# Kernel tuning notes

Hardware: AMD Instinct MI355X
Metric: run time of the kernel (lower is better)

Reference implementation:

```python
import jax, jax.numpy as jnp
import numpy as np

B, N, H, DH, E, D_IN = 2, 2048, 8, 32, 65536, 256
O = H * DH
SCALE = float(np.sqrt(DH))


def setup_inputs() -> dict:
    key = jax.random.key(0)
    ks = jax.random.split(key, 8)
    rng = np.random.default_rng(0)
    x = jax.random.normal(ks[0], (B, N, D_IN), jnp.float32)
    adj = jax.random.uniform(ks[1], (B, N, N), jnp.float32)
    # unique edges per graph so scatter-add matches torch advanced-index +=
    flat = np.stack([rng.choice(N * N, size=E, replace=False) for _ in range(B)])
    edge_index = jnp.asarray(np.stack([flat // N, flat % N], axis=1), jnp.int32)  # [B,2,E]
    edge_attr = jax.random.normal(ks[2], (B, E, H), jnp.float32)
    mask = jnp.ones((B, N), dtype=bool)
    qkv_w = jax.random.normal(ks[3], (D_IN, 3 * O), jnp.float32) / np.sqrt(D_IN)
    qkv_b = jnp.zeros((3 * O,), jnp.float32)
    e_w1 = jax.random.normal(ks[4], (H, H), jnp.float32) / np.sqrt(H)
    e_b1 = jnp.zeros((H,), jnp.float32)
    e_w2 = jax.random.normal(ks[5], (H, H), jnp.float32) / np.sqrt(H)
    e_b2 = jnp.zeros((H,), jnp.float32)
    shifts = jnp.asarray(np.linspace(0.1, 0.8, H), jnp.float32).reshape(1, H, 1, 1)
    widths = jnp.full((1, H, 1, 1), 0.5, jnp.float32)
    self_loop_W = jnp.asarray(1.0 / DH + rng.uniform(0, 1, H), jnp.float32).reshape(1, H, 1, 1)
    return dict(x=x, adj=adj, edge_attr=edge_attr, qkv_w=qkv_w, qkv_b=qkv_b,
                e_w1=e_w1, e_b1=e_b1, e_w2=e_w2, e_b2=e_b2,
                shifts=shifts, widths=widths, self_loop_W=self_loop_W,
                edge_index=edge_index, mask=mask)


def reference(x, adj, edge_attr, qkv_w, qkv_b, e_w1, e_b1, e_w2, e_b2,
              shifts, widths, self_loop_W, edge_index, mask):
    Bq, Nq = x.shape[0], x.shape[1]
    # qkv projection -> [3,B,H,N,DH]
    qkv = (x @ qkv_w + qkv_b).reshape(Bq, Nq, 3, H, DH)
    qkv = jnp.transpose(qkv, (2, 0, 3, 1, 4))
    Q, K, V = qkv[0], qkv[1], qkv[2]
    # edge FFN applied twice (eval mode: noise/dropout are identity)
    def ffn(e):
        return jax.nn.relu(e @ e_w1 + e_b1) @ e_w2 + e_b2
    ea = ffn(ffn(edge_attr))                      # [B,E,H]
    ea = jnp.transpose(ea, (0, 2, 1))             # [B,H,E]
    # scores + learned moire adjacency bias
    scores = jnp.einsum('bhqd,bhkd->bhqk', Q, K) / SCALE
    moire = jnp.exp(-((adj[:, None] - shifts) ** 2) / (2.0 * widths ** 2))  # gaussian focus
    moire = jnp.clip(moire, 1e-6, None)
    s = scores + jnp.log(moire)                   # [B,H,N,N]
    # scatter edge features into score matrix
    u = edge_index[:, 0, :]                        # [B,E]
    v = edge_index[:, 1, :]
    bi = jnp.arange(Bq)[:, None, None]
    hi = jnp.arange(H)[None, :, None]
    s = s.at[bi, hi, u[:, None, :], v[:, None, :]].add(ea)
    # self-loop diagonal bias (non-trainable)
    s = s + jnp.eye(Nq, dtype=s.dtype)[None, None] * self_loop_W
    # mask and softmax
    m2 = mask[:, None, :] & mask[:, :, None]       # [B,N,N]
    s = jnp.where(m2[:, None], s, jnp.asarray(-1e6, s.dtype))
    attn = jax.nn.softmax(s, axis=-1)
    out = jnp.einsum('bhqk,bhkd->bhqd', attn, V)
    return jnp.transpose(out, (0, 2, 1, 3)).reshape(Bq, Nq, O)
```

## Files before the change

### kernel.cpp

```cpp
#include <hip/hip_runtime.h>

#define B_ 2
#define N_ 2048
#define H_ 8
#define DH_ 32
#define E_ 65536
#define DIN_ 256
#define KT 256
#define NKT (N_ / KT)
#define ECAP 32
#define QSCALE 0.2550348872f
#define LOG2E 1.4426950408889634f
#define LOG2MIN -19.931568569324174f

typedef short bf16x8 __attribute__((ext_vector_type(8)));
typedef float floatx4 __attribute__((ext_vector_type(4)));

__device__ __forceinline__ unsigned short f2b(float f){
  union { float f; unsigned int u; } v; v.f = f;
  return (unsigned short)((v.u + 0x7fffu + ((v.u >> 16) & 1u)) >> 16);
}
__device__ __forceinline__ bf16x8 f8_to_bf(const float* p){
  float4 a = *(const float4*)p, b = *(const float4*)(p + 4);
  bf16x8 r;
  r[0] = (short)f2b(a.x); r[1] = (short)f2b(a.y); r[2] = (short)f2b(a.z); r[3] = (short)f2b(a.w);
  r[4] = (short)f2b(b.x); r[5] = (short)f2b(b.y); r[6] = (short)f2b(b.z); r[7] = (short)f2b(b.w);
  return r;
}
__device__ __forceinline__ unsigned int cvt_pk_bf16(float lo, float hi){
  unsigned int r;
  asm("v_cvt_pk_bf16_f32 %0, %1, %2" : "=v"(r) : "v"(lo), "v"(hi));
  return r;
}
__device__ __forceinline__ float fexp2(float x){
  float r;
  asm("v_exp_f32 %0, %1" : "=v"(r) : "v"(x));
  return r;
}

__global__ __launch_bounds__(256) void prep_kernel(
    const float* __restrict__ eattr,
    const float* __restrict__ w1, const float* __restrict__ b1,
    const float* __restrict__ w2, const float* __restrict__ b2,
    float* __restrict__ ea,
    const int* __restrict__ ei, int* __restrict__ cnt, unsigned int* __restrict__ pck,
    const float* __restrict__ w, unsigned short* __restrict__ wT,
    const float* __restrict__ x, unsigned short* __restrict__ xb)
{
  int bb = blockIdx.x, tid = threadIdx.x;
  if (bb < 512){
    __shared__ float W1[64], W2[64], Bv1[8], Bv2[8];
    if (tid < 64){ W1[tid] = w1[tid]; W2[tid] = w2[tid]; }
    if (tid < 8){ Bv1[tid] = b1[tid]; Bv2[tid] = b2[tid]; }
    __syncthreads();
    int gid = bb * 256 + tid;
    const float* ep = eattr + (size_t)gid * 8;
    float cur[8];
#pragma unroll
    for (int i = 0; i < 8; ++i) cur[i] = ep[i];
#pragma unroll
    for (int pass = 0; pass < 2; ++pass){
      float t[8];
#pragma unroll
      for (int j = 0; j < 8; ++j){
        float s = Bv1[j];
#pragma unroll
        for (int i = 0; i < 8; ++i) s += cur[i] * W1[i * 8 + j];
        t[j] = fmaxf(s, 0.f);
      }
#pragma unroll
      for (int j = 0; j < 8; ++j){
        float s = Bv2[j];
#pragma unroll
        for (int i = 0; i < 8; ++i) s += t[i] * W2[i * 8 + j];
        cur[j] = s;
      }
    }
    float* op = ea + (size_t)gid * 8;
#pragma unroll
    for (int j = 0; j < 8; ++j) op[j] = cur[j] * LOG2E;
  } else if (bb < 1024){
    int gid = (bb - 512) * 256 + tid;
    int b = gid >> 16, e = gid & (E_ - 1);
    int u = ei[(size_t)b * 2 * E_ + e];
    int v = ei[(size_t)b * 2 * E_ + E_ + e];
    int bucket = ((b << 11) + u) * 8 + (v >> 8);
    int slot = atomicAdd(&cnt[bucket], 1);
    if (slot < ECAP) pck[(size_t)bucket * ECAP + slot] = ((unsigned int)e << 11) | (unsigned int)v;
  } else if (bb < 1280){
    int k = bb - 1024;
    for (int c = tid; c < 768; c += 256)
      wT[(size_t)c * 256 + k] = f2b(w[(size_t)k * 768 + c]);
  } else {
    int gid = (bb - 1280) * 256 + tid;
    bf16x8 v = f8_to_bf(x + (size_t)gid * 8);
    *(bf16x8*)(xb + (size_t)gid * 8) = v;
  }
}

__global__ __launch_bounds__(256) void qkv_kernel(
    const unsigned short* __restrict__ xb, const unsigned short* __restrict__ wT,
    const float* __restrict__ bias,
    unsigned short* __restrict__ Qb, unsigned short* __restrict__ Kb, unsigned short* __restrict__ Vt)
{
  int tid = threadIdx.x;
  int wave = tid >> 6, lane = tid & 63, m = lane & 15, quad = lane >> 4;
  int rowbase = blockIdx.x * 16;
  int colbase = blockIdx.y * 64 + wave * 16;
  floatx4 acc = {0.f, 0.f, 0.f, 0.f};
#pragma unroll
  for (int kb = 0; kb < 8; ++kb){
    bf16x8 af = *(const bf16x8*)(xb + (size_t)(rowbase + m) * DIN_ + kb * 32 + quad * 8);
    bf16x8 bf = *(const bf16x8*)(wT + (size_t)(colbase + m) * DIN_ + kb * 32 + quad * 8);
    acc = __builtin_amdgcn_mfma_f32_16x16x32_bf16(af, bf, acc, 0, 0, 0);
  }
  int ccol = colbase + m;
  int which = ccol >> 8, hh = (ccol >> 5) & 7, dh = ccol & 31;
  float bv = bias[ccol];
  int row0 = rowbase + quad * 4;
  int bidx = row0 >> 11, n0 = row0 & (N_ - 1);
  size_t bh = (size_t)(bidx * H_ + hh);
  if (which == 0){
#pragma unroll
    for (int r = 0; r < 4; ++r)
      Qb[(bh * N_ + n0 + r) * DH_ + dh] = f2b((acc[r] + bv) * QSCALE);
  } else if (which == 1){
#pragma unroll
    for (int r = 0; r < 4; ++r)
      Kb[(bh * N_ + n0 + r) * DH_ + dh] = f2b(acc[r] + bv);
  } else {
    ushort4 st;
    st.x = f2b(acc[0] + bv); st.y = f2b(acc[1] + bv);
    st.z = f2b(acc[2] + bv); st.w = f2b(acc[3] + bv);
    *(ushort4*)(Vt + (bh * DH_ + dh) * N_ + n0) = st;
  }
}

__global__ __launch_bounds__(128) void attn_kernel(
    const unsigned short* __restrict__ Qb, const unsigned short* __restrict__ Kb,
    const unsigned short* __restrict__ Vt, const float* __restrict__ adj,
    const float* __restrict__ ea, const int* __restrict__ cnt, const unsigned int* __restrict__ pck,
    const float* __restrict__ shifts, const float* __restrict__ widths,
    const float* __restrict__ selfW, float* __restrict__ out)
{
  __shared__ float S[2][16][260];

  int bid = blockIdx.x;
  int xcd = bid & 7, t = bid >> 3;
  int hp = t & 3;
  int bqt = xcd * 32 + (t >> 2);
  int b = bqt >> 7, qt = bqt & 127;
  int qbase = qt * 16;
  int tid = threadIdx.x, wave = tid >> 6, lane = tid & 63, m = lane & 15, quad = lane >> 4;
  int h = hp * 2 + wave;
  float shift_h = shifts[h];
  float w_h = widths[h];
  float i2w_h = LOG2E / (2.f * w_h * w_h);
  float selfW_h = selfW[h] * LOG2E;
  size_t krow = (size_t)(b * H_ + h) * N_;
  size_t vrow = (size_t)(b * H_ + h) * DH_;
  bf16x8 qfrag = *(const bf16x8*)(Qb + (krow + qbase + m) * DH_ + quad * 8);
  float (*Sw)[260] = S[wave];

  int rr = lane >> 2, sl0 = lane & 3;
  const int* cntp = cnt + ((size_t)(b * N_) + qbase + rr) * 8;
  const unsigned int* pckp = pck + ((size_t)((b * N_ + qbase + rr) * 8)) * ECAP;
  const float* eabase = ea + (size_t)b * E_ * H_ + h;
  const float* adjp = adj + ((size_t)b * N_ + qbase + m) * N_ + quad * 8;
  const unsigned short* vp0 = Vt + (vrow + m) * N_ + quad * 8;
  const unsigned short* vp1 = Vt + (vrow + 16 + m) * N_ + quad * 8;
  const unsigned short* kp  = Kb + (krow + m) * DH_ + quad * 8;

  floatx4 sh4 = {shift_h, shift_h, shift_h, shift_h};
  floatx4 ni4 = {-i2w_h, -i2w_h, -i2w_h, -i2w_h};
  floatx4 lm4 = {LOG2MIN, LOG2MIN, LOG2MIN, LOG2MIN};
  floatx4 z4  = {0.f, 0.f, 0.f, 0.f};

  float mcur = -1e30f, lcur = 0.f;
  floatx4 oacc0 = z4, oacc1 = z4;

  int nb_c = cntp[0]; nb_c = nb_c > ECAP ? ECAP : nb_c;
  unsigned int pk0 = pckp[sl0];
  unsigned int pk1 = pckp[sl0 + 4];
  int vv0_c = (int)(pk0 & (N_ - 1));
  int vv1_c = (int)(pk1 & (N_ - 1));
  bool g0_c = (sl0 < nb_c);
  bool g1_c = (sl0 + 4 < nb_c);
  float ea0_c = 0.f, ea1_c = 0.f;
  if (g0_c) ea0_c = eabase[(size_t)(pk0 >> 11) * H_];
  if (g1_c) ea1_c = eabase[(size_t)(pk1 >> 11) * H_];

#pragma unroll 2
  for (int kt = 0; kt < NKT; ++kt){
    int k0 = kt * KT;
    int nb_n = 0; unsigned int pk0_n = 0, pk1_n = 0;
    if (kt + 1 < NKT){
      nb_n  = cntp[kt + 1];
      pk0_n = pckp[(kt + 1) * ECAP + sl0];
      pk1_n = pckp[(kt + 1) * ECAP + sl0 + 4];
    }
#pragma unroll
    for (int cb = 0; cb < 4; ++cb){
      const unsigned short* kpb = kp + (size_t)(k0 + cb * 64) * DH_;
#pragma unroll
      for (int s = 0; s < 4; ++s){
        bf16x8 kf = *(const bf16x8*)(kpb + (size_t)(s * 16) * DH_);
        floatx4 acc = __builtin_amdgcn_mfma_f32_16x16x32_bf16(qfrag, kf, z4, 0, 0, 0);
#pragma unroll
        for (int r = 0; r < 4; ++r)
          Sw[quad * 4 + r][cb * 64 + s * 16 + m] = acc[r];
      }
    }
    {
      int dw = qbase - k0;
      if ((unsigned)dw < 256u && lane < 16)
        Sw[lane][dw + lane] += selfW_h;
    }
    if (g0_c) Sw[rr][vv0_c - k0] += ea0_c;
    if (g1_c) Sw[rr][vv1_c - k0] += ea1_c;
    if (nb_c > 8){
      for (int slot = sl0 + 8; slot < nb_c; slot += 4){
        unsigned int p = pckp[kt * ECAP + slot];
        Sw[rr][(int)(p & (N_ - 1)) - k0] += eabase[(size_t)(p >> 11) * H_];
      }
    }
    int vv0_n = 0, vv1_n = 0; bool g0_n = false, g1_n = false;
    float ea0_n = 0.f, ea1_n = 0.f;
    if (kt + 1 < NKT){
      nb_n = nb_n > ECAP ? ECAP : nb_n;
      vv0_n = (int)(pk0_n & (N_ - 1));
      vv1_n = (int)(pk1_n & (N_ - 1));
      g0_n = (sl0 < nb_n);
      g1_n = (sl0 + 4 < nb_n);
      if (g0_n) ea0_n = eabase[(size_t)(pk0_n >> 11) * H_];
      if (g1_n) ea1_n = eabase[(size_t)(pk1_n >> 11) * H_];
    }
    floatx4 sv[4][4];
#pragma unroll
    for (int cb = 0; cb < 4; ++cb){
      const float* sp = &Sw[m][cb * 64 + quad * 8];
      sv[cb][0] = *(const floatx4*)(sp);
      sv[cb][1] = *(const floatx4*)(sp + 4);
      sv[cb][2] = *(const floatx4*)(sp + 32);
      sv[cb][3] = *(const floatx4*)(sp + 36);
      const float* ap = adjp + k0 + cb * 64;
      floatx4 a0 = *(const floatx4*)(ap);
      floatx4 a1 = *(const floatx4*)(ap + 4);
      floatx4 a2 = *(const floatx4*)(ap + 32);
      floatx4 a3 = *(const floatx4*)(ap + 36);
      floatx4 d;
      d = a0 - sh4; sv[cb][0] += __builtin_elementwise_max(d * d * ni4, lm4);
      d = a1 - sh4; sv[cb][1] += __builtin_elementwise_max(d * d * ni4, lm4);
      d = a2 - sh4; sv[cb][2] += __builtin_elementwise_max(d * d * ni4, lm4);
      d = a3 - sh4; sv[cb][3] += __builtin_elementwise_max(d * d * ni4, lm4);
    }
    floatx4 mx01 = __builtin_elementwise_max(
        __builtin_elementwise_max(sv[0][0], sv[0][1]),
        __builtin_elementwise_max(sv[0][2], sv[0][3]));
    floatx4 mx23 = __builtin_elementwise_max(
        __builtin_elementwise_max(sv[1][0], sv[1][1]),
        __builtin_elementwise_max(sv[1][2], sv[1][3]));
    floatx4 mx45 = __builtin_elementwise_max(
        __builtin_elementwise_max(sv[2][0], sv[2][1]),
        __builtin_elementwise_max(sv[2][2], sv[2][3]));
    floatx4 mx67 = __builtin_elementwise_max(
        __builtin_elementwise_max(sv[3][0], sv[3][1]),
        __builtin_elementwise_max(sv[3][2], sv[3][3]));
    floatx4 mxv = __builtin_elementwise_max(__builtin_elementwise_max(mx01, mx23),
                                            __builtin_elementwise_max(mx45, mx67));
    float lm = fmaxf(fmaxf(mxv.x, mxv.y), fmaxf(mxv.z, mxv.w));
    lm = fmaxf(lm, __shfl_xor(lm, 16));
    lm = fmaxf(lm, __shfl_xor(lm, 32));
    float mnew = fmaxf(mcur, lm);
    float al = fexp2(mcur - mnew);
    mcur = mnew;
    float al0 = __shfl(al, quad * 4 + 0);
    float al1 = __shfl(al, quad * 4 + 1);
    float al2 = __shfl(al, quad * 4 + 2);
    float al3 = __shfl(al, quad * 4 + 3);
    oacc0[0] *= al0; oacc0[1] *= al1; oacc0[2] *= al2; oacc0[3] *= al3;
    oacc1[0] *= al0; oacc1[1] *= al1; oacc1[2] *= al2; oacc1[3] *= al3;
    floatx4 m4 = {mcur, mcur, mcur, mcur};
    floatx4 psv = z4;
#pragma unroll
    for (int cb = 0; cb < 4; ++cb){
      const unsigned short* vA = vp0 + k0 + cb * 64;
      const unsigned short* vB = vp1 + k0 + cb * 64;
      bf16x8 vf00 = *(const bf16x8*)(vA);
      bf16x8 vf01 = *(const bf16x8*)(vB);
      bf16x8 vf10 = *(const bf16x8*)(vA + 32);
      bf16x8 vf11 = *(const bf16x8*)(vB + 32);
      floatx4 e0 = sv[cb][0] - m4, e1 = sv[cb][1] - m4;
      floatx4 e2 = sv[cb][2] - m4, e3 = sv[cb][3] - m4;
      floatx4 p0, p1, p2, p3;
      p0.x = fexp2(e0.x); p0.y = fexp2(e0.y); p0.z = fexp2(e0.z); p0.w = fexp2(e0.w);
      p1.x = fexp2(e1.x); p1.y = fexp2(e1.y); p1.z = fexp2(e1.z); p1.w = fexp2(e1.w);
      p2.x = fexp2(e2.x); p2.y = fexp2(e2.y); p2.z = fexp2(e2.z); p2.w = fexp2(e2.w);
      p3.x = fexp2(e3.x); p3.y = fexp2(e3.y); p3.z = fexp2(e3.z); p3.w = fexp2(e3.w);
      psv += (p0 + p1) + (p2 + p3);
      union { bf16x8 v; unsigned int u[4]; } PL, PH;
      PL.u[0] = cvt_pk_bf16(p0.x, p0.y); PL.u[1] = cvt_pk_bf16(p0.z, p0.w);
      PL.u[2] = cvt_pk_bf16(p1.x, p1.y); PL.u[3] = cvt_pk_bf16(p1.z, p1.w);
      PH.u[0] = cvt_pk_bf16(p2.x, p2.y); PH.u[1] = cvt_pk_bf16(p2.z, p2.w);
      PH.u[2] = cvt_pk_bf16(p3.x, p3.y); PH.u[3] = cvt_pk_bf16(p3.z, p3.w);
      oacc0 = __builtin_amdgcn_mfma_f32_16x16x32_bf16(PL.v, vf00, oacc0, 0, 0, 0);
      oacc1 = __builtin_amdgcn_mfma_f32_16x16x32_bf16(PL.v, vf01, oacc1, 0, 0, 0);
      oacc0 = __builtin_amdgcn_mfma_f32_16x16x32_bf16(PH.v, vf10, oacc0, 0, 0, 0);
      oacc1 = __builtin_amdgcn_mfma_f32_16x16x32_bf16(PH.v, vf11, oacc1, 0, 0, 0);
    }
    float ps = (psv.x + psv.y) + (psv.z + psv.w);
    ps += __shfl_xor(ps, 16);
    ps += __shfl_xor(ps, 32);
    lcur = lcur * al + ps;
    nb_c = nb_n; g0_c = g0_n; g1_c = g1_n;
    vv0_c = vv0_n; vv1_c = vv1_n; ea0_c = ea0_n; ea1_c = ea1_n;
  }

  float linv0 = 1.f / __shfl(lcur, quad * 4 + 0);
  float linv1 = 1.f / __shfl(lcur, quad * 4 + 1);
  float linv2 = 1.f / __shfl(lcur, quad * 4 + 2);
  float linv3 = 1.f / __shfl(lcur, quad * 4 + 3);
  float* ob = out + ((size_t)b * N_ + qbase + quad * 4) * (H_ * DH_) + h * DH_;
  ob[0 * H_ * DH_ + m]      = oacc0[0] * linv0;
  ob[0 * H_ * DH_ + 16 + m] = oacc1[0] * linv0;
  ob[1 * H_ * DH_ + m]      = oacc0[1] * linv1;
  ob[1 * H_ * DH_ + 16 + m] = oacc1[1] * linv1;
  ob[2 * H_ * DH_ + m]      = oacc0[2] * linv2;
  ob[2 * H_ * DH_ + 16 + m] = oacc1[2] * linv2;
  ob[3 * H_ * DH_ + m]      = oacc0[3] * linv3;
  ob[3 * H_ * DH_ + 16 + m] = oacc1[3] * linv3;
}

extern "C" void kernel_launch(void* const* d_in, const int* in_sizes, int n_in,
                              void* d_out, int out_size, void* d_ws, size_t ws_size,
                              hipStream_t stream)
{
  const float* x      = (const float*)d_in[0];
  const float* adj    = (const float*)d_in[1];
  const float* eattr  = (const float*)d_in[2];
  const float* qkvw   = (const float*)d_in[3];
  const float* qkvb   = (const float*)d_in[4];
  const float* ew1    = (const float*)d_in[5];
  const float* eb1    = (const float*)d_in[6];
  const float* ew2    = (const float*)d_in[7];
  const float* eb2    = (const float*)d_in[8];
  const float* shifts = (const float*)d_in[9];
  const float* widths = (const float*)d_in[10];
  const float* selfW  = (const float*)d_in[11];
  const int*   ei     = (const int*)d_in[12];
  float* out = (float*)d_out;

  char* ws = (char*)d_ws;
  unsigned short* Qb  = (unsigned short*)(ws);
  unsigned short* Kb  = (unsigned short*)(ws + ((size_t)2 << 20));
  unsigned short* Vt  = (unsigned short*)(ws + ((size_t)4 << 20));
  unsigned short* wT  = (unsigned short*)(ws + ((size_t)6 << 20));
  float*          ea  = (float*)(ws + ((size_t)7 << 20));
  int*            cnt = (int*)(ws + ((size_t)11 << 20));
  unsigned int*  pck  = (unsigned int*)(ws + ((size_t)12 << 20));
  unsigned short* xb  = (unsigned short*)(ws + ((size_t)16 << 20));

  hipMemsetAsync(cnt, 0, (size_t)B_ * N_ * 8 * sizeof(int), stream);
  hipLaunchKernelGGL(prep_kernel, dim3(1792), dim3(256), 0, stream,
                     eattr, ew1, eb1, ew2, eb2, ea, ei, cnt, pck, qkvw, wT, x, xb);
  hipLaunchKernelGGL(qkv_kernel, dim3(256, 12), dim3(256), 0, stream, xb, wT, qkvb, Qb, Kb, Vt);
  hipLaunchKernelGGL(attn_kernel, dim3(B_ * (H_ / 2) * (N_ / 16)), dim3(128), 0, stream,
                     Qb, Kb, Vt, adj, ea, cnt, pck, shifts, widths, selfW, out);
}
```

Baseline: 210.1 us.

## Split key range across two waves per head with flash-decoding style merge

Each block now runs four waves instead of two, so each head's key sequence is split into two halves processed by separate waves. The partial max, sum and output are merged through shared memory after a block barrier. To fit four waves, the per-wave score scratch is halved to 128 columns and each 256-key tile is processed in two sub-passes. This doubles the parallelism per query tile and shortens each wave's serial loop, at the cost of a final reduction, a barrier, and recomputation of the edge-slot filter per sub-pass.

```diff
diff --git a/kernel.cpp b/kernel.cpp
--- a/kernel.cpp
+++ b/kernel.cpp
@@ -7,7 +7,6 @@
 #define E_ 65536
 #define DIN_ 256
 #define KT 256
-#define NKT (N_ / KT)
 #define ECAP 32
 #define QSCALE 0.2550348872f
 #define LOG2E 1.4426950408889634f
@@ -136,14 +135,15 @@
   }
 }
 
-__global__ __launch_bounds__(128) void attn_kernel(
+__global__ __launch_bounds__(256) void attn_kernel(
     const unsigned short* __restrict__ Qb, const unsigned short* __restrict__ Kb,
     const unsigned short* __restrict__ Vt, const float* __restrict__ adj,
     const float* __restrict__ ea, const int* __restrict__ cnt, const unsigned int* __restrict__ pck,
     const float* __restrict__ shifts, const float* __restrict__ widths,
     const float* __restrict__ selfW, float* __restrict__ out)
 {
-  __shared__ float S[2][16][260];
+  __shared__ float S[4][16][132];
+  __shared__ float mfin[4][16], lfin[4][16];
 
   int bid = blockIdx.x;
   int xcd = bid & 7, t = bid >> 3;
@@ -152,7 +152,8 @@
   int b = bqt >> 7, qt = bqt & 127;
   int qbase = qt * 16;
   int tid = threadIdx.x, wave = tid >> 6, lane = tid & 63, m = lane & 15, quad = lane >> 4;
-  int h = hp * 2 + wave;
+  int hs = wave & 1, kh = wave >> 1;
+  int h = hp * 2 + hs;
   float shift_h = shifts[h];
   float w_h = widths[h];
   float i2w_h = LOG2E / (2.f * w_h * w_h);
@@ -160,7 +161,7 @@
   size_t krow = (size_t)(b * H_ + h) * N_;
   size_t vrow = (size_t)(b * H_ + h) * DH_;
   bf16x8 qfrag = *(const bf16x8*)(Qb + (krow + qbase + m) * DH_ + quad * 8);
-  float (*Sw)[260] = S[wave];
+  float (*Sw)[132] = S[wave];
 
   int rr = lane >> 2, sl0 = lane & 3;
   const int* cntp = cnt + ((size_t)(b * N_) + qbase + rr) * 8;
@@ -179,9 +180,10 @@
   float mcur = -1e30f, lcur = 0.f;
   floatx4 oacc0 = z4, oacc1 = z4;
 
-  int nb_c = cntp[0]; nb_c = nb_c > ECAP ? ECAP : nb_c;
-  unsigned int pk0 = pckp[sl0];
-  unsigned int pk1 = pckp[sl0 + 4];
+  int ktg0 = kh * 4;
+  int nb_c = cntp[ktg0]; nb_c = nb_c > ECAP ? ECAP : nb_c;
+  unsigned int pk0 = pckp[ktg0 * ECAP + sl0];
+  unsigned int pk1 = pckp[ktg0 * ECAP + sl0 + 4];
   int vv0_c = (int)(pk0 & (N_ - 1));
   int vv1_c = (int)(pk1 & (N_ - 1));
   bool g0_c = (sl0 < nb_c);
@@ -190,43 +192,68 @@
   if (g0_c) ea0_c = eabase[(size_t)(pk0 >> 11) * H_];
   if (g1_c) ea1_c = eabase[(size_t)(pk1 >> 11) * H_];
 
-#pragma unroll 2
-  for (int kt = 0; kt < NKT; ++kt){
-    int k0 = kt * KT;
+  for (int kt = 0; kt < 4; ++kt){
+    int ktg = ktg0 + kt;
+    int k0 = ktg * KT;
     int nb_n = 0; unsigned int pk0_n = 0, pk1_n = 0;
-    if (kt + 1 < NKT){
-      nb_n  = cntp[kt + 1];
-      pk0_n = pckp[(kt + 1) * ECAP + sl0];
-      pk1_n = pckp[(kt + 1) * ECAP + sl0 + 4];
-    }
-#pragma unroll
-    for (int cb = 0; cb < 4; ++cb){
-      const unsigned short* kpb = kp + (size_t)(k0 + cb * 64) * DH_;
-#pragma unroll
-      for (int s = 0; s < 4; ++s){
-        bf16x8 kf = *(const bf16x8*)(kpb + (size_t)(s * 16) * DH_);
-        floatx4 acc = __builtin_amdgcn_mfma_f32_16x16x32_bf16(qfrag, kf, z4, 0, 0, 0);
-#pragma unroll
-        for (int r = 0; r < 4; ++r)
-          Sw[quad * 4 + r][cb * 64 + s * 16 + m] = acc[r];
-      }
-    }
-    {
-      int dw = qbase - k0;
-      if ((unsigned)dw < 256u && lane < 16)
-        Sw[lane][dw + lane] += selfW_h;
-    }
-    if (g0_c) Sw[rr][vv0_c - k0] += ea0_c;
-    if (g1_c) Sw[rr][vv1_c - k0] += ea1_c;
-    if (nb_c > 8){
-      for (int slot = sl0 + 8; slot < nb_c; slot += 4){
-        unsigned int p = pckp[kt * ECAP + slot];
-        Sw[rr][(int)(p & (N_ - 1)) - k0] += eabase[(size_t)(p >> 11) * H_];
+    if (kt + 1 < 4){
+      nb_n  = cntp[ktg + 1];
+      pk0_n = pckp[(ktg + 1) * ECAP + sl0];
+      pk1_n = pckp[(ktg + 1) * ECAP + sl0 + 4];
+    }
+    floatx4 sv[4][4];
+#pragma unroll
+    for (int p = 0; p < 2; ++p){
+      int kw = k0 + p * 128;
+#pragma unroll
+      for (int cb = 0; cb < 2; ++cb){
+        const unsigned short* kpb = kp + (size_t)(kw + cb * 64) * DH_;
+#pragma unroll
+        for (int s = 0; s < 4; ++s){
+          bf16x8 kf = *(const bf16x8*)(kpb + (size_t)(s * 16) * DH_);
+          floatx4 acc = __builtin_amdgcn_mfma_f32_16x16x32_bf16(qfrag, kf, z4, 0, 0, 0);
+#pragma unroll
+          for (int r = 0; r < 4; ++r)
+            Sw[quad * 4 + r][cb * 64 + s * 16 + m] = acc[r];
+        }
+      }
+      {
+        int dw = qbase - kw;
+        if ((unsigned)dw < 128u && lane < 16)
+          Sw[lane][dw + lane] += selfW_h;
+      }
+      if (g0_c && ((vv0_c - k0) >> 7) == p) Sw[rr][(vv0_c - k0) & 127] += ea0_c;
+      if (g1_c && ((vv1_c - k0) >> 7) == p) Sw[rr][(vv1_c - k0) & 127] += ea1_c;
+      if (nb_c > 8){
+        for (int slot = sl0 + 8; slot < nb_c; slot += 4){
+          unsigned int pkx = pckp[ktg * ECAP + slot];
+          int c = (int)(pkx & (N_ - 1)) - k0;
+          if ((c >> 7) == p) Sw[rr][c & 127] += eabase[(size_t)(pkx >> 11) * H_];
+        }
+      }
+#pragma unroll
+      for (int cb = 0; cb < 2; ++cb){
+        int g = p * 2 + cb;
+        const float* sp = &Sw[m][cb * 64 + quad * 8];
+        sv[g][0] = *(const floatx4*)(sp);
+        sv[g][1] = *(const floatx4*)(sp + 4);
+        sv[g][2] = *(const floatx4*)(sp + 32);
+        sv[g][3] = *(const floatx4*)(sp + 36);
+        const float* ap = adjp + kw + cb * 64;
+        floatx4 a0 = *(const floatx4*)(ap);
+        floatx4 a1 = *(const floatx4*)(ap + 4);
+        floatx4 a2 = *(const floatx4*)(ap + 32);
+        floatx4 a3 = *(const floatx4*)(ap + 36);
+        floatx4 d;
+        d = a0 - sh4; sv[g][0] += __builtin_elementwise_max(d * d * ni4, lm4);
+        d = a1 - sh4; sv[g][1] += __builtin_elementwise_max(d * d * ni4, lm4);
+        d = a2 - sh4; sv[g][2] += __builtin_elementwise_max(d * d * ni4, lm4);
+        d = a3 - sh4; sv[g][3] += __builtin_elementwise_max(d * d * ni4, lm4);
       }
     }
     int vv0_n = 0, vv1_n = 0; bool g0_n = false, g1_n = false;
     float ea0_n = 0.f, ea1_n = 0.f;
-    if (kt + 1 < NKT){
+    if (kt + 1 < 4){
       nb_n = nb_n > ECAP ? ECAP : nb_n;
       vv0_n = (int)(pk0_n & (N_ - 1));
       vv1_n = (int)(pk1_n & (N_ - 1));
@@ -234,25 +261,6 @@
       g1_n = (sl0 + 4 < nb_n);
       if (g0_n) ea0_n = eabase[(size_t)(pk0_n >> 11) * H_];
       if (g1_n) ea1_n = eabase[(size_t)(pk1_n >> 11) * H_];
-    }
-    floatx4 sv[4][4];
-#pragma unroll
-    for (int cb = 0; cb < 4; ++cb){
-      const float* sp = &Sw[m][cb * 64 + quad * 8];
-      sv[cb][0] = *(const floatx4*)(sp);
-      sv[cb][1] = *(const floatx4*)(sp + 4);
-      sv[cb][2] = *(const floatx4*)(sp + 32);
-      sv[cb][3] = *(const floatx4*)(sp + 36);
-      const float* ap = adjp + k0 + cb * 64;
-      floatx4 a0 = *(const floatx4*)(ap);
-      floatx4 a1 = *(const floatx4*)(ap + 4);
-      floatx4 a2 = *(const floatx4*)(ap + 32);
-      floatx4 a3 = *(const floatx4*)(ap + 36);
-      floatx4 d;
-      d = a0 - sh4; sv[cb][0] += __builtin_elementwise_max(d * d * ni4, lm4);
-      d = a1 - sh4; sv[cb][1] += __builtin_elementwise_max(d * d * ni4, lm4);
-      d = a2 - sh4; sv[cb][2] += __builtin_elementwise_max(d * d * ni4, lm4);
-      d = a3 - sh4; sv[cb][3] += __builtin_elementwise_max(d * d * ni4, lm4);
     }
     floatx4 mx01 = __builtin_elementwise_max(
         __builtin_elementwise_max(sv[0][0], sv[0][1]),
@@ -268,10 +276,10 @@
         __builtin_elementwise_max(sv[3][2], sv[3][3]));
     floatx4 mxv = __builtin_elementwise_max(__builtin_elementwise_max(mx01, mx23),
                                             __builtin_elementwise_max(mx45, mx67));
-    float lm = fmaxf(fmaxf(mxv.x, mxv.y), fmaxf(mxv.z, mxv.w));
-    lm = fmaxf(lm, __shfl_xor(lm, 16));
-    lm = fmaxf(lm, __shfl_xor(lm, 32));
-    float mnew = fmaxf(mcur, lm);
+    float lmx = fmaxf(fmaxf(mxv.x, mxv.y), fmaxf(mxv.z, mxv.w));
+    lmx = fmaxf(lmx, __shfl_xor(lmx, 16));
+    lmx = fmaxf(lmx, __shfl_xor(lmx, 32));
+    float mnew = fmaxf(mcur, lmx);
     float al = fexp2(mcur - mnew);
     mcur = mnew;
     float al0 = __shfl(al, quad * 4 + 0);
@@ -283,15 +291,15 @@
     floatx4 m4 = {mcur, mcur, mcur, mcur};
     floatx4 psv = z4;
 #pragma unroll
-    for (int cb = 0; cb < 4; ++cb){
-      const unsigned short* vA = vp0 + k0 + cb * 64;
-      const unsigned short* vB = vp1 + k0 + cb * 64;
+    for (int g = 0; g < 4; ++g){
+      const unsigned short* vA = vp0 + k0 + g * 64;
+      const unsigned short* vB = vp1 + k0 + g * 64;
       bf16x8 vf00 = *(const bf16x8*)(vA);
       bf16x8 vf01 = *(const bf16x8*)(vB);
       bf16x8 vf10 = *(const bf16x8*)(vA + 32);
       bf16x8 vf11 = *(const bf16x8*)(vB + 32);
-      floatx4 e0 = sv[cb][0] - m4, e1 = sv[cb][1] - m4;
-      floatx4 e2 = sv[cb][2] - m4, e3 = sv[cb][3] - m4;
+      floatx4 e0 = sv[g][0] - m4, e1 = sv[g][1] - m4;
+      floatx4 e2 = sv[g][2] - m4, e3 = sv[g][3] - m4;
       floatx4 p0, p1, p2, p3;
       p0.x = fexp2(e0.x); p0.y = fexp2(e0.y); p0.z = fexp2(e0.z); p0.w = fexp2(e0.w);
       p1.x = fexp2(e1.x); p1.y = fexp2(e1.y); p1.z = fexp2(e1.z); p1.w = fexp2(e1.w);
@@ -316,19 +324,25 @@
     vv0_c = vv0_n; vv1_c = vv1_n; ea0_c = ea0_n; ea1_c = ea1_n;
   }
 
-  float linv0 = 1.f / __shfl(lcur, quad * 4 + 0);
-  float linv1 = 1.f / __shfl(lcur, quad * 4 + 1);
-  float linv2 = 1.f / __shfl(lcur, quad * 4 + 2);
-  float linv3 = 1.f / __shfl(lcur, quad * 4 + 3);
-  float* ob = out + ((size_t)b * N_ + qbase + quad * 4) * (H_ * DH_) + h * DH_;
-  ob[0 * H_ * DH_ + m]      = oacc0[0] * linv0;
-  ob[0 * H_ * DH_ + 16 + m] = oacc1[0] * linv0;
-  ob[1 * H_ * DH_ + m]      = oacc0[1] * linv1;
-  ob[1 * H_ * DH_ + 16 + m] = oacc1[1] * linv1;
-  ob[2 * H_ * DH_ + m]      = oacc0[2] * linv2;
-  ob[2 * H_ * DH_ + 16 + m] = oacc1[2] * linv2;
-  ob[3 * H_ * DH_ + m]      = oacc0[3] * linv3;
-  ob[3 * H_ * DH_ + 16 + m] = oacc1[3] * linv3;
+  if (quad == 0){ mfin[wave][m] = mcur; lfin[wave][m] = lcur; }
+  float* Ow = &S[wave][0][0];
+#pragma unroll
+  for (int r = 0; r < 4; ++r){
+    Ow[(quad * 4 + r) * 132 + m]      = oacc0[r];
+    Ow[(quad * 4 + r) * 132 + 16 + m] = oacc1[r];
+  }
+  __syncthreads();
+#pragma unroll
+  for (int ii = 0; ii < 4; ++ii){
+    int i = tid + ii * 256;
+    int hs2 = i >> 9, r = (i >> 5) & 15, d = i & 31;
+    float m0 = mfin[hs2][r], m1 = mfin[hs2 + 2][r];
+    float mg = fmaxf(m0, m1);
+    float w0 = fexp2(m0 - mg), w1 = fexp2(m1 - mg);
+    float o = S[hs2][r][d] * w0 + S[hs2 + 2][r][d] * w1;
+    float l = lfin[hs2][r] * w0 + lfin[hs2 + 2][r] * w1;
+    out[((size_t)b * N_ + qbase + r) * (H_ * DH_) + (hp * 2 + hs2) * DH_ + d] = o / l;
+  }
 }
 
 extern "C" void kernel_launch(void* const* d_in, const int* in_sizes, int n_in,
@@ -364,6 +378,6 @@
   hipLaunchKernelGGL(prep_kernel, dim3(1792), dim3(256), 0, stream,
                      eattr, ew1, eb1, ew2, eb2, ea, ei, cnt, pck, qkvw, wT, x, xb);
   hipLaunchKernelGGL(qkv_kernel, dim3(256, 12), dim3(256), 0, stream, xb, wT, qkvb, Qb, Kb, Vt);
-  hipLaunchKernelGGL(attn_kernel, dim3(B_ * (H_ / 2) * (N_ / 16)), dim3(128), 0, stream,
+  hipLaunchKernelGGL(attn_kernel, dim3(B_ * (H_ / 2) * (N_ / 16)), dim3(256), 0, stream,
                      Qb, Kb, Vt, adj, ea, cnt, pck, shifts, widths, selfW, out);
 }
```

After: 217.6 us. +3.6%, slower.
